# Kernel tuning notes

Hardware: AMD Instinct MI355X
Metric: run time of the kernel (lower is better)

## Reference

```python
import jax, jax.numpy as jnp
import numpy as np

GRID = 16  # int(sqrt(num_patches=256))
# fixed ragged grid shapes: 32 images cycling through 4 aspect ratios
_SHAPES = np.array([[32, 32], [16, 64], [24, 40], [40, 24]] * 8, dtype=np.int64)  # [32,2]
_SIZES = _SHAPES[:, 0] * _SHAPES[:, 1]  # per-image patch counts
_SEQ_LEN = int(_SIZES.sum())  # 31744


def setup_inputs() -> dict:
    key = jax.random.key(0)
    k1, k2, k3 = jax.random.split(key, 3)
    return {
        "seq_patches": jax.random.normal(k1, (_SEQ_LEN, 768), dtype=jnp.float32),
        "w": jax.random.normal(k2, (1152, 768), dtype=jnp.float32) * 0.02,
        "b": jnp.zeros((1152,), dtype=jnp.float32),
        "pos_emb": jax.random.normal(k3, (256, 1152), dtype=jnp.float32) * 0.02,
        "seq_sizes": jnp.asarray(_SIZES),
        "spatial_shapes": jnp.asarray(_SHAPES),
    }


def reference(seq_patches, w, b, pos_emb, seq_sizes, spatial_shapes):
    # Linear patch embedding: [S, 768] @ [768, 1152] + [1152]
    patch_embeds = seq_patches @ w.T + b
    d = pos_emb.shape[-1]
    pos_grid = pos_emb.reshape(GRID, GRID, d)  # [16,16,D]
    shapes = np.asarray(spatial_shapes)  # static host-side shapes (ragged loop)
    pos_list = []
    for h, wd in shapes:
        # antialiased bilinear resize, half-pixel centers (align_corners=False)
        rp = jax.image.resize(pos_grid, (int(h), int(wd), d), method="linear", antialias=True)
        pos_list.append(rp.reshape(int(h) * int(wd), d))
    pos_embeds = jnp.concatenate(pos_list, axis=0)  # [S, D]
    return patch_embeds + pos_embeds
```

## Files before the change

kernel.cpp:

```cpp
#include <hip/hip_runtime.h>
#include <hip/hip_bf16.h>
#include <cstdint>
#include <cstddef>

typedef __attribute__((ext_vector_type(8))) short short8;
typedef __attribute__((ext_vector_type(4))) float f32x4;

static constexpr int M_TOT = 31744;
static constexpr int N_TOT = 1152;
static constexpr int K_TOT = 768;
static constexpr long A_ELEMS = (long)M_TOT * K_TOT;
static constexpr long W_ELEMS = (long)N_TOT * K_TOT;
static constexpr int CYC_ROWS = 3968;

__device__ __forceinline__ unsigned short f2bf(float f) {
  unsigned int u = __float_as_uint(f);
  u += 0x7FFFu + ((u >> 16) & 1u);
  return (unsigned short)(u >> 16);
}
__device__ __forceinline__ float bf2f(unsigned short u) {
  return __uint_as_float((unsigned int)u << 16);
}

__global__ void cvt_kernel(const float* __restrict__ A, const float* __restrict__ W,
                           unsigned short* __restrict__ dst) {
  long chunk = (long)blockIdx.x * blockDim.x + threadIdx.x;
  long i = chunk * 8;
  const float* src = (i < A_ELEMS) ? (A + i) : (W + (i - A_ELEMS));
  float4 v0 = *(const float4*)(src);
  float4 v1 = *(const float4*)(src + 4);
  short8 o;
  o[0] = (short)f2bf(v0.x); o[1] = (short)f2bf(v0.y);
  o[2] = (short)f2bf(v0.z); o[3] = (short)f2bf(v0.w);
  o[4] = (short)f2bf(v1.x); o[5] = (short)f2bf(v1.y);
  o[6] = (short)f2bf(v1.z); o[7] = (short)f2bf(v1.w);
  *(short8*)(dst + i) = o;
}

__global__ void tab_kernel(const float* __restrict__ pos, const float* __restrict__ bias,
                           unsigned short* __restrict__ tab) {
  const int t = blockIdx.x * blockDim.x + threadIdx.x;
  const int row = t / 144;
  const int dc = (t - row * 144) * 8;

  int rr, cc; float sy, sx;
  if (row < 1024)      { rr = row >> 5; cc = row & 31; sy = 0.5f;         sx = 0.5f; }
  else if (row < 2048) { const int li = row - 1024; rr = li >> 6; cc = li & 63; sy = 1.0f; sx = 0.25f; }
  else if (row < 3008) { const int li = row - 2048; rr = li / 40; cc = li - rr * 40; sy = 16.0f / 24.0f; sx = 0.4f; }
  else                 { const int li = row - 3008; rr = li / 24; cc = li - rr * 24; sy = 0.4f; sx = 16.0f / 24.0f; }
  float yc = fminf(fmaxf(((float)rr + 0.5f) * sy - 0.5f, 0.0f), 15.0f);
  const int y0 = (int)yc; const float fy = yc - (float)y0;
  const int y1 = y0 < 15 ? y0 + 1 : 15;
  float xc = fminf(fmaxf(((float)cc + 0.5f) * sx - 0.5f, 0.0f), 15.0f);
  const int x0 = (int)xc; const float fx = xc - (float)x0;
  const int x1 = x0 < 15 ? x0 + 1 : 15;
  const float w11 = fy * fx;
  const float w10 = fy - w11;
  const float w01 = fx - w11;
  const float w00 = 1.0f - fy - fx + w11;
  const float* p00 = pos + (size_t)(y0 * 16 + x0) * 1152 + dc;
  const float* p01 = pos + (size_t)(y0 * 16 + x1) * 1152 + dc;
  const float* p10 = pos + (size_t)(y1 * 16 + x0) * 1152 + dc;
  const float* p11 = pos + (size_t)(y1 * 16 + x1) * 1152 + dc;
  const float* bi  = bias + dc;
  short8 o;
#pragma unroll
  for (int j = 0; j < 8; ++j) {
    const float v = bi[j] + w00 * p00[j] + w01 * p01[j] + w10 * p10[j] + w11 * p11[j];
    o[j] = (short)f2bf(v);
  }
  *(short8*)(tab + (size_t)row * 1152 + dc) = o;
}

__device__ __forceinline__ void gload_lds16(const void* g, void* l) {
  __builtin_amdgcn_global_load_lds((__attribute__((address_space(1))) void*)g,
                                   (__attribute__((address_space(3))) void*)l, 16, 0, 0);
}

__global__ __launch_bounds__(256) void gemm_kernel(
    const unsigned short* __restrict__ Abf, const unsigned short* __restrict__ Wbf,
    const unsigned short* __restrict__ tab, float* __restrict__ outp) {
  __shared__ __attribute__((aligned(16))) unsigned short As[128 * 64];
  __shared__ __attribute__((aligned(16))) unsigned short Bs[128 * 64];

  const int bid = blockIdx.x;
  const int tile = (bid & 7) * 279 + (bid >> 3);
  const int tm = tile / 9, tn = tile % 9;
  const int m0 = tm * 128, n0 = tn * 128;

  const int tid = threadIdx.x;
  const int wid = tid >> 6, lane = tid & 63;
  const int wr = wid >> 1, wc = wid & 1;
  const int rb = wid * 32;
  const int lrow = lane >> 3;
  const int lcol = ((lane & 7) ^ lrow) * 8;

  f32x4 acc[4][4] = {};

  const unsigned short* Abase = Abf + (size_t)m0 * K_TOT;
  const unsigned short* Bbase = Wbf + (size_t)n0 * K_TOT;

  for (int kt = 0; kt < 12; ++kt) {
    const int k0 = kt * 64;
#pragma unroll
    for (int c = 0; c < 4; ++c) {
      const int row = rb + c * 8;
      gload_lds16(Abase + (size_t)(row + lrow) * K_TOT + k0 + lcol,
                  (char*)As + row * 128);
      gload_lds16(Bbase + (size_t)(row + lrow) * K_TOT + k0 + lcol,
                  (char*)Bs + row * 128);
    }
    __syncthreads();

    const int kg = lane >> 4;
#pragma unroll
    for (int kk = 0; kk < 2; ++kk) {
      short8 fa[4], fb[4];
#pragma unroll
      for (int m = 0; m < 4; ++m) {
        const int arow = wr * 64 + m * 16 + (lane & 15);
        const int ab = arow * 128 + (((kk * 4 + kg) ^ (arow & 7)) << 4);
        fa[m] = *(const short8*)((const char*)As + ab);
      }
#pragma unroll
      for (int n = 0; n < 4; ++n) {
        const int brow = wc * 64 + n * 16 + (lane & 15);
        const int bb = brow * 128 + (((kk * 4 + kg) ^ (brow & 7)) << 4);
        fb[n] = *(const short8*)((const char*)Bs + bb);
      }
#pragma unroll
      for (int m = 0; m < 4; ++m)
#pragma unroll
        for (int n = 0; n < 4; ++n)
          acc[m][n] = __builtin_amdgcn_mfma_f32_16x16x32_bf16(fa[m], fb[n], acc[m][n], 0, 0, 0);
    }
    __syncthreads();
  }

  const int s_base = m0 + wr * 64 + ((lane >> 4) << 2);
  const int rem_base = s_base % CYC_ROWS;
  const int d_base = n0 + wc * 64 + (lane & 15);

#pragma unroll
  for (int m = 0; m < 4; ++m) {
#pragma unroll
    for (int r = 0; r < 4; ++r) {
      const int off = m * 16 + r;
      int rem = rem_base + off;
      if (rem >= CYC_ROWS) rem -= CYC_ROWS;
      const unsigned short* trow = tab + (size_t)rem * 1152 + d_base;
      float* orow = outp + (size_t)(s_base + off) * 1152 + d_base;
#pragma unroll
      for (int n = 0; n < 4; ++n)
        orow[n * 16] = acc[m][n][r] + bf2f(trow[n * 16]);
    }
  }
}

extern "C" void kernel_launch(void* const* d_in, const int* in_sizes, int n_in,
                              void* d_out, int out_size, void* d_ws, size_t ws_size,
                              hipStream_t stream) {
  const float* A    = (const float*)d_in[0];
  const float* W    = (const float*)d_in[1];
  const float* bias = (const float*)d_in[2];
  const float* pos  = (const float*)d_in[3];
  unsigned short* Abf = (unsigned short*)d_ws;
  unsigned short* Wbf = Abf + A_ELEMS;
  unsigned short* tab = Wbf + W_ELEMS;
  float* outp = (float*)d_out;

  cvt_kernel<<<12336, 256, 0, stream>>>(A, W, Abf);
  tab_kernel<<<2232, 256, 0, stream>>>(pos, bias, tab);
  gemm_kernel<<<2232, 256, 0, stream>>>(Abf, Wbf, tab, outp);
}
```

Measured before the change: 127.9 us.

## Triple-buffer GEMM LDS loads with 256x128 tiles and 512-thread blocks

Restructures the bf16 GEMM to use 256x128 output tiles with 8 waves per block and a three-stage LDS ring buffer. Global-to-LDS loads for tile t+2 are issued before computing tile t, with explicit vmcnt waits and one barrier per k-step in place of two. The aim is to hide global load latency and cut synchronisation, and the larger tile improves B reuse. In exchange it uses more LDS (144KB per block), which may limit occupancy, and the XCD tile remap is adjusted for the new tile count.

```diff
diff --git a/kernel.cpp b/kernel.cpp
--- a/kernel.cpp
+++ b/kernel.cpp
@@ -77,69 +77,97 @@
                                    (__attribute__((address_space(3))) void*)l, 16, 0, 0);
 }
 
-__global__ __launch_bounds__(256) void gemm_kernel(
+__global__ __launch_bounds__(512, 2) void gemm_kernel(
     const unsigned short* __restrict__ Abf, const unsigned short* __restrict__ Wbf,
     const unsigned short* __restrict__ tab, float* __restrict__ outp) {
-  __shared__ __attribute__((aligned(16))) unsigned short As[128 * 64];
-  __shared__ __attribute__((aligned(16))) unsigned short Bs[128 * 64];
+  __shared__ __attribute__((aligned(16))) unsigned short As[3][256 * 64];
+  __shared__ __attribute__((aligned(16))) unsigned short Bs[3][128 * 64];
 
   const int bid = blockIdx.x;
-  const int tile = (bid & 7) * 279 + (bid >> 3);
-  const int tm = tile / 9, tn = tile % 9;
-  const int m0 = tm * 128, n0 = tn * 128;
+  const int xcd = bid & 7, idx = bid >> 3;
+  const int wgid = (xcd < 4 ? xcd * 140 : 560 + (xcd - 4) * 139) + idx;
+  const int tm = wgid / 9, tn = wgid - tm * 9;
+  const int m0 = tm * 256, n0 = tn * 128;
 
   const int tid = threadIdx.x;
-  const int wid = tid >> 6, lane = tid & 63;
-  const int wr = wid >> 1, wc = wid & 1;
-  const int rb = wid * 32;
-  const int lrow = lane >> 3;
-  const int lcol = ((lane & 7) ^ lrow) * 8;
+  const int w = tid >> 6, lane = tid & 63;
+  const int wr = w >> 1, wc = w & 1;
+
+  const int rowc = tid >> 3;
+  const int chunk8 = (((tid & 7) ^ (rowc & 7)) << 3);
+  const int wbase = w << 10;
+
+  const unsigned short* Abase = Abf + (size_t)m0 * K_TOT + chunk8 + (size_t)rowc * K_TOT;
+  const unsigned short* Bbase = Wbf + (size_t)n0 * K_TOT + chunk8 + (size_t)rowc * K_TOT;
 
   f32x4 acc[4][4] = {};
 
-  const unsigned short* Abase = Abf + (size_t)m0 * K_TOT;
-  const unsigned short* Bbase = Wbf + (size_t)n0 * K_TOT;
-
-  for (int kt = 0; kt < 12; ++kt) {
-    const int k0 = kt * 64;
-#pragma unroll
-    for (int c = 0; c < 4; ++c) {
-      const int row = rb + c * 8;
-      gload_lds16(Abase + (size_t)(row + lrow) * K_TOT + k0 + lcol,
-                  (char*)As + row * 128);
-      gload_lds16(Bbase + (size_t)(row + lrow) * K_TOT + k0 + lcol,
-                  (char*)Bs + row * 128);
+  const int kg = lane >> 4;
+  const int l15 = lane & 15;
+
+#define STAGE(tt)                                                                 \
+  {                                                                               \
+    const int buf_ = (tt) % 3;                                                    \
+    const int k0_ = (tt) * 64;                                                    \
+    char* Ab_ = (char*)As[buf_];                                                  \
+    char* Bb_ = (char*)Bs[buf_];                                                  \
+    gload_lds16(Abase + (size_t)0 * K_TOT + k0_,   Ab_ + 0     + wbase);          \
+    gload_lds16(Abase + (size_t)64 * K_TOT + k0_,  Ab_ + 8192  + wbase);          \
+    gload_lds16(Abase + (size_t)128 * K_TOT + k0_, Ab_ + 16384 + wbase);          \
+    gload_lds16(Abase + (size_t)192 * K_TOT + k0_, Ab_ + 24576 + wbase);          \
+    gload_lds16(Bbase + (size_t)0 * K_TOT + k0_,   Bb_ + 0     + wbase);          \
+    gload_lds16(Bbase + (size_t)64 * K_TOT + k0_,  Bb_ + 8192  + wbase);          \
+  }
+
+#define COMPUTE(tt)                                                               \
+  {                                                                               \
+    const int buf_ = (tt) % 3;                                                    \
+    const char* Ab_ = (const char*)As[buf_];                                      \
+    const char* Bb_ = (const char*)Bs[buf_];                                      \
+    short8 fb[4][2];                                                              \
+    _Pragma("unroll") for (int n = 0; n < 4; ++n) {                               \
+      const int brow = wc * 64 + n * 16 + l15;                                    \
+      _Pragma("unroll") for (int kk = 0; kk < 2; ++kk)                            \
+        fb[n][kk] = *(const short8*)(Bb_ + brow * 128 +                           \
+                                     (((kk * 4 + kg) ^ (brow & 7)) << 4));        \
+    }                                                                             \
+    _Pragma("unroll") for (int mh = 0; mh < 2; ++mh) {                            \
+      short8 fa[2][2];                                                            \
+      _Pragma("unroll") for (int m = 0; m < 2; ++m) {                             \
+        const int arow = wr * 64 + (mh * 2 + m) * 16 + l15;                       \
+        _Pragma("unroll") for (int kk = 0; kk < 2; ++kk)                          \
+          fa[m][kk] = *(const short8*)(Ab_ + arow * 128 +                         \
+                                       (((kk * 4 + kg) ^ (arow & 7)) << 4));      \
+      }                                                                           \
+      _Pragma("unroll") for (int m = 0; m < 2; ++m)                               \
+        _Pragma("unroll") for (int n = 0; n < 4; ++n)                             \
+          _Pragma("unroll") for (int kk = 0; kk < 2; ++kk)                        \
+            acc[mh * 2 + m][n] = __builtin_amdgcn_mfma_f32_16x16x32_bf16(         \
+                fa[m][kk], fb[n][kk], acc[mh * 2 + m][n], 0, 0, 0);               \
+    }                                                                             \
+  }
+
+  STAGE(0)
+  STAGE(1)
+  asm volatile("s_waitcnt vmcnt(6)" ::: "memory");
+  __builtin_amdgcn_s_barrier();
+
+#pragma unroll
+  for (int t = 0; t < 12; ++t) {
+    if (t < 10) STAGE(t + 2)
+    COMPUTE(t)
+    if (t < 11) {
+      if (t < 10) { asm volatile("s_waitcnt vmcnt(6)" ::: "memory"); }
+      else        { asm volatile("s_waitcnt vmcnt(0)" ::: "memory"); }
+      __builtin_amdgcn_s_barrier();
     }
-    __syncthreads();
-
-    const int kg = lane >> 4;
-#pragma unroll
-    for (int kk = 0; kk < 2; ++kk) {
-      short8 fa[4], fb[4];
-#pragma unroll
-      for (int m = 0; m < 4; ++m) {
-        const int arow = wr * 64 + m * 16 + (lane & 15);
-        const int ab = arow * 128 + (((kk * 4 + kg) ^ (arow & 7)) << 4);
-        fa[m] = *(const short8*)((const char*)As + ab);
-      }
-#pragma unroll
-      for (int n = 0; n < 4; ++n) {
-        const int brow = wc * 64 + n * 16 + (lane & 15);
-        const int bb = brow * 128 + (((kk * 4 + kg) ^ (brow & 7)) << 4);
-        fb[n] = *(const short8*)((const char*)Bs + bb);
-      }
-#pragma unroll
-      for (int m = 0; m < 4; ++m)
-#pragma unroll
-        for (int n = 0; n < 4; ++n)
-          acc[m][n] = __builtin_amdgcn_mfma_f32_16x16x32_bf16(fa[m], fb[n], acc[m][n], 0, 0, 0);
-    }
-    __syncthreads();
-  }
+  }
+#undef STAGE
+#undef COMPUTE
 
   const int s_base = m0 + wr * 64 + ((lane >> 4) << 2);
   const int rem_base = s_base % CYC_ROWS;
-  const int d_base = n0 + wc * 64 + (lane & 15);
+  const int d_base = n0 + wc * 64 + l15;
 
 #pragma unroll
   for (int m = 0; m < 4; ++m) {
@@ -171,5 +199,5 @@
 
   cvt_kernel<<<12336, 256, 0, stream>>>(A, W, Abf);
   tab_kernel<<<2232, 256, 0, stream>>>(pos, bias, tab);
-  gemm_kernel<<<2232, 256, 0, stream>>>(Abf, Wbf, tab, outp);
-}
+  gemm_kernel<<<1116, 512, 0, stream>>>(Abf, Wbf, tab, outp);
+}
```

Result: slower. 151.4 us (+18.4%).

## Rewrite GEMM as 256x256-tile, 8-wave double-buffered pipeline with interleaved loads

Applied to the files above, without the earlier changes.

The GEMM kernel moves from 128x128 tiles with 4 waves and a single LDS buffer to 256x256 tiles with 8 waves per block. LDS is double-buffered, and global-to-LDS loads for the next K step are interleaved with MFMA quadrants using explicit vmcnt waits, barriers and setprio. The goal is to hide memory latency and raise operand reuse per block. The cost is much higher register and LDS use (128 KB LDS). Because N=1152 is not a multiple of 256, the last column tile pads by clamping B rows and skips stores for out-of-range wave columns, and the XCD-aware remap of tiles to blocks also changes.

```diff
diff --git a/kernel.cpp b/kernel.cpp
--- a/kernel.cpp
+++ b/kernel.cpp
@@ -77,82 +77,138 @@
                                    (__attribute__((address_space(3))) void*)l, 16, 0, 0);
 }
 
-__global__ __launch_bounds__(256) void gemm_kernel(
+__global__ __launch_bounds__(512, 2) void gemm_kernel(
     const unsigned short* __restrict__ Abf, const unsigned short* __restrict__ Wbf,
     const unsigned short* __restrict__ tab, float* __restrict__ outp) {
-  __shared__ __attribute__((aligned(16))) unsigned short As[128 * 64];
-  __shared__ __attribute__((aligned(16))) unsigned short Bs[128 * 64];
+  __shared__ __attribute__((aligned(16))) unsigned short As[2][256 * 64];
+  __shared__ __attribute__((aligned(16))) unsigned short Bs[2][256 * 64];
 
   const int bid = blockIdx.x;
-  const int tile = (bid & 7) * 279 + (bid >> 3);
-  const int tm = tile / 9, tn = tile % 9;
-  const int m0 = tm * 128, n0 = tn * 128;
+  const int xcd = bid & 7, idx = bid >> 3;
+  const int wgid = (xcd < 4 ? xcd * 78 : 312 + (xcd - 4) * 77) + idx;
+  const int tm = wgid / 5, tn = wgid - tm * 5;
+  const int m0 = tm * 256, n0 = tn * 256;
 
   const int tid = threadIdx.x;
-  const int wid = tid >> 6, lane = tid & 63;
-  const int wr = wid >> 1, wc = wid & 1;
-  const int rb = wid * 32;
-  const int lrow = lane >> 3;
-  const int lcol = ((lane & 7) ^ lrow) * 8;
-
-  f32x4 acc[4][4] = {};
-
-  const unsigned short* Abase = Abf + (size_t)m0 * K_TOT;
-  const unsigned short* Bbase = Wbf + (size_t)n0 * K_TOT;
-
-  for (int kt = 0; kt < 12; ++kt) {
-    const int k0 = kt * 64;
-#pragma unroll
-    for (int c = 0; c < 4; ++c) {
-      const int row = rb + c * 8;
-      gload_lds16(Abase + (size_t)(row + lrow) * K_TOT + k0 + lcol,
-                  (char*)As + row * 128);
-      gload_lds16(Bbase + (size_t)(row + lrow) * K_TOT + k0 + lcol,
-                  (char*)Bs + row * 128);
+  const int w = tid >> 6, lane = tid & 63;
+  const int wm = w >> 2, wn = w & 3;
+  const int lr = lane >> 3;
+  const int csw = ((lane & 7) ^ lr) << 3;
+  const int kg = lane >> 4, l15 = lane & 15;
+
+  const unsigned short* Ab0 = Abf + (size_t)(m0 + w * 8 + lr) * K_TOT + csw;
+  const int a_wu = w << 10;
+  const int brow_lane = (w & 3) * 8 + lr;
+  const int b_ws = (w >> 2) * 64;
+  const int b_wu = (w & 3) << 10;
+
+  f32x4 acc[8][4] = {};
+  short8 fa[4][2];
+  short8 fb[2][2][2];
+
+#define STAGE_A(p, t1, H)                                                        \
+  { gload_lds16(Ab0 + (size_t)((H) * 64) * K_TOT + (t1) * 64,                    \
+                (char*)As[p] + ((H) * 64) * 128 + a_wu);                         \
+    gload_lds16(Ab0 + (size_t)((H) * 64 + 128) * K_TOT + (t1) * 64,              \
+                (char*)As[p] + ((H) * 64 + 128) * 128 + a_wu); }
+
+#define STAGE_B(p, t1, NQ)                                                       \
+  { const int sb0_ = (NQ) * 32 + b_ws;                                           \
+    int br0_ = n0 + sb0_ + brow_lane; if (br0_ > N_TOT - 1) br0_ = N_TOT - 1;    \
+    gload_lds16(Wbf + (size_t)br0_ * K_TOT + csw + (t1) * 64,                    \
+                (char*)Bs[p] + sb0_ * 128 + b_wu);                               \
+    const int sb1_ = sb0_ + 128;                                                 \
+    int br1_ = n0 + sb1_ + brow_lane; if (br1_ > N_TOT - 1) br1_ = N_TOT - 1;    \
+    gload_lds16(Wbf + (size_t)br1_ * K_TOT + csw + (t1) * 64,                    \
+                (char*)Bs[p] + sb1_ * 128 + b_wu); }
+
+#define LOAD_FA(p, MQ)                                                           \
+  _Pragma("unroll") for (int j = 0; j < 4; ++j) {                                \
+    const int ar_ = wm * 128 + (MQ) * 64 + j * 16 + l15;                         \
+    const char* ba_ = (const char*)As[p] + ar_ * 128;                            \
+    fa[j][0] = *(const short8*)(ba_ + ((kg ^ (ar_ & 7)) << 4));                  \
+    fa[j][1] = *(const short8*)(ba_ + (((4 + kg) ^ (ar_ & 7)) << 4));            \
+  }
+
+#define LOAD_FB(p, NQ)                                                           \
+  _Pragma("unroll") for (int j = 0; j < 2; ++j) {                                \
+    const int br_ = wn * 64 + (NQ) * 32 + j * 16 + l15;                          \
+    const char* bb_ = (const char*)Bs[p] + br_ * 128;                            \
+    fb[NQ][j][0] = *(const short8*)(bb_ + ((kg ^ (br_ & 7)) << 4));              \
+    fb[NQ][j][1] = *(const short8*)(bb_ + (((4 + kg) ^ (br_ & 7)) << 4));        \
+  }
+
+#define MFMA_Q(MQ, NQ)                                                           \
+  _Pragma("unroll") for (int j = 0; j < 4; ++j)                                  \
+    _Pragma("unroll") for (int jj = 0; jj < 2; ++jj) {                           \
+      acc[(MQ) * 4 + j][(NQ) * 2 + jj] = __builtin_amdgcn_mfma_f32_16x16x32_bf16(\
+          fa[j][0], fb[NQ][jj][0], acc[(MQ) * 4 + j][(NQ) * 2 + jj], 0, 0, 0);   \
+      acc[(MQ) * 4 + j][(NQ) * 2 + jj] = __builtin_amdgcn_mfma_f32_16x16x32_bf16(\
+          fa[j][1], fb[NQ][jj][1], acc[(MQ) * 4 + j][(NQ) * 2 + jj], 0, 0, 0);   \
     }
-    __syncthreads();
-
-    const int kg = lane >> 4;
-#pragma unroll
-    for (int kk = 0; kk < 2; ++kk) {
-      short8 fa[4], fb[4];
-#pragma unroll
-      for (int m = 0; m < 4; ++m) {
-        const int arow = wr * 64 + m * 16 + (lane & 15);
-        const int ab = arow * 128 + (((kk * 4 + kg) ^ (arow & 7)) << 4);
-        fa[m] = *(const short8*)((const char*)As + ab);
+
+#define BAR __builtin_amdgcn_s_barrier()
+#define SP1 __builtin_amdgcn_s_setprio(1)
+#define SP0 __builtin_amdgcn_s_setprio(0)
+#define VM4 asm volatile("s_waitcnt vmcnt(4)" ::: "memory")
+#define VM2 asm volatile("s_waitcnt vmcnt(2)" ::: "memory")
+#define VM0 asm volatile("s_waitcnt vmcnt(0)" ::: "memory")
+
+  STAGE_A(0, 0, 0)
+  STAGE_B(0, 0, 0)
+  STAGE_B(0, 0, 1)
+  STAGE_A(0, 0, 1)
+  VM4;
+  BAR;
+
+#pragma unroll
+  for (int t = 0; t < 11; ++t) {
+    const int p = t & 1, q = p ^ 1;
+    LOAD_FA(p, 0) LOAD_FB(p, 0)
+    STAGE_A(q, t + 1, 0)
+    VM4; BAR; SP1; MFMA_Q(0, 0) SP0; BAR;
+    LOAD_FB(p, 1)
+    STAGE_B(q, t + 1, 0)
+    VM4; BAR; SP1; MFMA_Q(0, 1) SP0; BAR;
+    LOAD_FA(p, 1)
+    STAGE_B(q, t + 1, 1)
+    BAR; SP1; MFMA_Q(1, 0) SP0; BAR;
+    STAGE_A(q, t + 1, 1)
+    VM4; BAR; SP1; MFMA_Q(1, 1) SP0; BAR;
+    __builtin_amdgcn_sched_barrier(0);
+  }
+
+  LOAD_FA(1, 0) LOAD_FB(1, 0)
+  VM2; BAR; SP1; MFMA_Q(0, 0) SP0; BAR;
+  LOAD_FB(1, 1)
+  VM0; BAR; SP1; MFMA_Q(0, 1) SP0; BAR;
+  LOAD_FA(1, 1)
+  BAR; SP1; MFMA_Q(1, 0) SP0; BAR;
+  SP1; MFMA_Q(1, 1) SP0;
+
+#undef STAGE_A
+#undef STAGE_B
+#undef LOAD_FA
+#undef LOAD_FB
+#undef MFMA_Q
+
+  const int s_base = m0 + wm * 128 + ((lane >> 4) << 2);
+  const int rem_base = s_base % CYC_ROWS;
+  const int d_base = n0 + wn * 64 + l15;
+  if (n0 + wn * 64 < N_TOT) {
+#pragma unroll
+    for (int fm = 0; fm < 8; ++fm) {
+#pragma unroll
+      for (int r = 0; r < 4; ++r) {
+        const int off = fm * 16 + r;
+        int rem = rem_base + off;
+        if (rem >= CYC_ROWS) rem -= CYC_ROWS;
+        const unsigned short* trow = tab + (size_t)rem * 1152 + d_base;
+        float* orow = outp + (size_t)(s_base + off) * 1152 + d_base;
+#pragma unroll
+        for (int fn = 0; fn < 4; ++fn)
+          orow[fn * 16] = acc[fm][fn][r] + bf2f(trow[fn * 16]);
       }
-#pragma unroll
-      for (int n = 0; n < 4; ++n) {
-        const int brow = wc * 64 + n * 16 + (lane & 15);
-        const int bb = brow * 128 + (((kk * 4 + kg) ^ (brow & 7)) << 4);
-        fb[n] = *(const short8*)((const char*)Bs + bb);
-      }
-#pragma unroll
-      for (int m = 0; m < 4; ++m)
-#pragma unroll
-        for (int n = 0; n < 4; ++n)
-          acc[m][n] = __builtin_amdgcn_mfma_f32_16x16x32_bf16(fa[m], fb[n], acc[m][n], 0, 0, 0);
-    }
-    __syncthreads();
-  }
-
-  const int s_base = m0 + wr * 64 + ((lane >> 4) << 2);
-  const int rem_base = s_base % CYC_ROWS;
-  const int d_base = n0 + wc * 64 + (lane & 15);
-
-#pragma unroll
-  for (int m = 0; m < 4; ++m) {
-#pragma unroll
-    for (int r = 0; r < 4; ++r) {
-      const int off = m * 16 + r;
-      int rem = rem_base + off;
-      if (rem >= CYC_ROWS) rem -= CYC_ROWS;
-      const unsigned short* trow = tab + (size_t)rem * 1152 + d_base;
-      float* orow = outp + (size_t)(s_base + off) * 1152 + d_base;
-#pragma unroll
-      for (int n = 0; n < 4; ++n)
-        orow[n * 16] = acc[m][n][r] + bf2f(trow[n * 16]);
     }
   }
 }
@@ -171,5 +227,5 @@
 
   cvt_kernel<<<12336, 256, 0, stream>>>(A, W, Abf);
   tab_kernel<<<2232, 256, 0, stream>>>(pos, bias, tab);
-  gemm_kernel<<<2232, 256, 0, stream>>>(Abf, Wbf, tab, outp);
-}
+  gemm_kernel<<<620, 512, 0, stream>>>(Abf, Wbf, tab, outp);
+}
```

Result: no change. 126.9 us (-0.8%).

## Double-buffer GEMM LDS tiles to overlap global loads with MFMA compute

Applied to the files above, without the earlier changes.

The GEMM main loop now uses two LDS buffers for A and B. The next K-tile is loaded asynchronously via global_load_lds while MFMAs run on the current tile, with one barrier per iteration instead of two. Wave priority is raised around the MFMA block. LDS use doubles to 64 KB per block, which may reduce occupancy on the CU.

```diff
diff --git a/kernel.cpp b/kernel.cpp
--- a/kernel.cpp
+++ b/kernel.cpp
@@ -80,8 +80,8 @@
 __global__ __launch_bounds__(256) void gemm_kernel(
     const unsigned short* __restrict__ Abf, const unsigned short* __restrict__ Wbf,
     const unsigned short* __restrict__ tab, float* __restrict__ outp) {
-  __shared__ __attribute__((aligned(16))) unsigned short As[128 * 64];
-  __shared__ __attribute__((aligned(16))) unsigned short Bs[128 * 64];
+  __shared__ __attribute__((aligned(16))) unsigned short As[2][128 * 64];
+  __shared__ __attribute__((aligned(16))) unsigned short Bs[2][128 * 64];
 
   const int bid = blockIdx.x;
   const int tile = (bid & 7) * 279 + (bid >> 3);
@@ -94,52 +94,64 @@
   const int rb = wid * 32;
   const int lrow = lane >> 3;
   const int lcol = ((lane & 7) ^ lrow) * 8;
+  const int kg = lane >> 4, l15 = lane & 15;
 
   f32x4 acc[4][4] = {};
 
   const unsigned short* Abase = Abf + (size_t)m0 * K_TOT;
   const unsigned short* Bbase = Wbf + (size_t)n0 * K_TOT;
 
-  for (int kt = 0; kt < 12; ++kt) {
-    const int k0 = kt * 64;
+#define STAGE(p, kt)                                                             \
+  { const int k0_ = (kt) * 64;                                                   \
+    _Pragma("unroll") for (int c = 0; c < 4; ++c) {                              \
+      const int row_ = rb + c * 8;                                               \
+      gload_lds16(Abase + (size_t)(row_ + lrow) * K_TOT + k0_ + lcol,            \
+                  (char*)As[p] + row_ * 128);                                    \
+      gload_lds16(Bbase + (size_t)(row_ + lrow) * K_TOT + k0_ + lcol,            \
+                  (char*)Bs[p] + row_ * 128);                                    \
+    } }
+
+#define COMPUTE(p)                                                               \
+  { __builtin_amdgcn_s_setprio(1);                                               \
+    _Pragma("unroll") for (int kk = 0; kk < 2; ++kk) {                           \
+      short8 fa[4], fb[4];                                                       \
+      _Pragma("unroll") for (int m = 0; m < 4; ++m) {                            \
+        const int arow = wr * 64 + m * 16 + l15;                                 \
+        fa[m] = *(const short8*)((const char*)As[p] + arow * 128 +               \
+                                 (((kk * 4 + kg) ^ (arow & 7)) << 4));           \
+      }                                                                          \
+      _Pragma("unroll") for (int n = 0; n < 4; ++n) {                            \
+        const int brow = wc * 64 + n * 16 + l15;                                 \
+        fb[n] = *(const short8*)((const char*)Bs[p] + brow * 128 +               \
+                                 (((kk * 4 + kg) ^ (brow & 7)) << 4));           \
+      }                                                                          \
+      _Pragma("unroll") for (int m = 0; m < 4; ++m)                              \
+        _Pragma("unroll") for (int n = 0; n < 4; ++n)                            \
+          acc[m][n] = __builtin_amdgcn_mfma_f32_16x16x32_bf16(                   \
+              fa[m], fb[n], acc[m][n], 0, 0, 0);                                 \
+    }                                                                            \
+    __builtin_amdgcn_s_setprio(0); }
+
+  STAGE(0, 0)
+  asm volatile("s_waitcnt vmcnt(0)" ::: "memory");
+  __builtin_amdgcn_s_barrier();
+
 #pragma unroll
-    for (int c = 0; c < 4; ++c) {
-      const int row = rb + c * 8;
-      gload_lds16(Abase + (size_t)(row + lrow) * K_TOT + k0 + lcol,
-                  (char*)As + row * 128);
-      gload_lds16(Bbase + (size_t)(row + lrow) * K_TOT + k0 + lcol,
-                  (char*)Bs + row * 128);
-    }
-    __syncthreads();
+  for (int t = 0; t < 11; ++t) {
+    const int p = t & 1, q = p ^ 1;
+    STAGE(q, t + 1)
+    COMPUTE(p)
+    asm volatile("s_waitcnt vmcnt(0)" ::: "memory");
+    __builtin_amdgcn_s_barrier();
+  }
+  COMPUTE(1)
 
-    const int kg = lane >> 4;
-#pragma unroll
-    for (int kk = 0; kk < 2; ++kk) {
-      short8 fa[4], fb[4];
-#pragma unroll
-      for (int m = 0; m < 4; ++m) {
-        const int arow = wr * 64 + m * 16 + (lane & 15);
-        const int ab = arow * 128 + (((kk * 4 + kg) ^ (arow & 7)) << 4);
-        fa[m] = *(const short8*)((const char*)As + ab);
-      }
-#pragma unroll
-      for (int n = 0; n < 4; ++n) {
-        const int brow = wc * 64 + n * 16 + (lane & 15);
-        const int bb = brow * 128 + (((kk * 4 + kg) ^ (brow & 7)) << 4);
-        fb[n] = *(const short8*)((const char*)Bs + bb);
-      }
-#pragma unroll
-      for (int m = 0; m < 4; ++m)
-#pragma unroll
-        for (int n = 0; n < 4; ++n)
-          acc[m][n] = __builtin_amdgcn_mfma_f32_16x16x32_bf16(fa[m], fb[n], acc[m][n], 0, 0, 0);
-    }
-    __syncthreads();
-  }
+#undef STAGE
+#undef COMPUTE
 
   const int s_base = m0 + wr * 64 + ((lane >> 4) << 2);
   const int rem_base = s_base % CYC_ROWS;
-  const int d_base = n0 + wc * 64 + (lane & 15);
+  const int d_base = n0 + wc * 64 + l15;
 
 #pragma unroll
   for (int m = 0; m < 4; ++m) {
```

Measured after the change: 118.0 us. 7.7% less time.
